# Kernel optimization log

Measured on AMD Instinct MI355X. Metric: run time of the kernel, lower is better.

Reference implementation:

```python
import jax, jax.numpy as jnp
import numpy as np

D_MODEL = 1024
N_HEADS = 16
D_HEAD = D_MODEL // N_HEADS
D_FF = 4096
EPS = 1e-5


def layernorm(x, gamma, beta):
    mu = jnp.mean(x, axis=-1, keepdims=True)
    var = jnp.var(x, axis=-1, keepdims=True)
    return (x - mu) * jax.lax.rsqrt(var + EPS) * gamma + beta


def setup_inputs() -> dict:
    key = jax.random.key(0)
    ks = jax.random.split(key, 16)
    B, T = 4, 2048
    s = 1.0 / np.sqrt(D_MODEL)
    sf = 1.0 / np.sqrt(D_FF)
    return {
        "x": jax.random.normal(ks[0], (B, T, D_MODEL), jnp.float32),
        "gate_score": jax.random.uniform(ks[1], (B,), jnp.float32),
        "Wq": jax.random.normal(ks[2], (D_MODEL, D_MODEL), jnp.float32) * s,
        "bq": jnp.zeros((D_MODEL,), jnp.float32),
        "Wk": jax.random.normal(ks[3], (D_MODEL, D_MODEL), jnp.float32) * s,
        "bk": jnp.zeros((D_MODEL,), jnp.float32),
        "Wv": jax.random.normal(ks[4], (D_MODEL, D_MODEL), jnp.float32) * s,
        "bv": jnp.zeros((D_MODEL,), jnp.float32),
        "Wo": jax.random.normal(ks[5], (D_MODEL, D_MODEL), jnp.float32) * s,
        "bo": jnp.zeros((D_MODEL,), jnp.float32),
        "W1": jax.random.normal(ks[6], (D_MODEL, D_FF), jnp.float32) * s,
        "b1": jnp.zeros((D_FF,), jnp.float32),
        "W2": jax.random.normal(ks[7], (D_FF, D_MODEL), jnp.float32) * sf,
        "b2": jnp.zeros((D_MODEL,), jnp.float32),
        "gamma1": jnp.ones((D_MODEL,), jnp.float32),
        "beta1": jnp.zeros((D_MODEL,), jnp.float32),
        "gamma2": jnp.ones((D_MODEL,), jnp.float32),
        "beta2": jnp.zeros((D_MODEL,), jnp.float32),
    }


def reference(x, gate_score, Wq, bq, Wk, bk, Wv, bv, Wo, bo,
              W1, b1, W2, b2, gamma1, beta1, gamma2, beta2):
    B, T, C = x.shape
    # --- attention sub-block (pre-norm) ---
    h = layernorm(x, gamma1, beta1)
    Q = (h @ Wq + bq).reshape(B, T, N_HEADS, D_HEAD).transpose(0, 2, 1, 3)
    K = (h @ Wk + bk).reshape(B, T, N_HEADS, D_HEAD).transpose(0, 2, 1, 3)
    V = (h @ Wv + bv).reshape(B, T, N_HEADS, D_HEAD).transpose(0, 2, 1, 3)
    scores = jnp.einsum("bhqd,bhkd->bhqk", Q, K) / np.sqrt(D_HEAD)
    causal = jnp.tril(jnp.ones((T, T), dtype=bool))  # True = keep
    scores = jnp.where(causal, scores, -jnp.inf)
    attn = jax.nn.softmax(scores, axis=-1)
    ctx = jnp.einsum("bhqk,bhkd->bhqd", attn, V)
    ctx = ctx.transpose(0, 2, 1, 3).reshape(B, T, C)
    attn_out = ctx @ Wo + bo
    x1 = x + attn_out
    # --- FFN sub-block (pre-norm) ---
    h2 = layernorm(x1, gamma2, beta2)
    ff = jax.nn.gelu(h2 @ W1 + b1, approximate=False) @ W2 + b2
    x2 = x1 + ff
    # --- gated residual ---
    g = gate_score[:, None, None]
    return x + g * (x2 - x)
```

## Files before the change

kernel.cpp:

```cpp
#include <hip/hip_runtime.h>
#include <hip/hip_bf16.h>
#include <cmath>

typedef unsigned short u16;
typedef __attribute__((ext_vector_type(8))) short short8;
typedef __attribute__((ext_vector_type(4))) float f32x4;

#define DM 1024
#define NH 16
#define DH 64
#define DFF 4096
#define BB 4
#define TT 2048
#define MROWS (BB*TT)

__device__ __forceinline__ float bu2f(u16 u) {
    union { float f; unsigned v; } c; c.v = ((unsigned)u) << 16; return c.f;
}
__device__ __forceinline__ u16 f2bu(float f) {
    __hip_bfloat16 h = __float2bfloat16(f);
    union { __hip_bfloat16 h; u16 u; } c; c.h = h; return c.u;
}
__device__ __forceinline__ void async_copy16(const u16* g, u16* l) {
    __builtin_amdgcn_global_load_lds((const __attribute__((address_space(1))) void*)g,
                                     (__attribute__((address_space(3))) void*)l, 16, 0, 0);
}

__global__ void ln_kernel(const float* __restrict__ x, const float* __restrict__ gamma,
                          const float* __restrict__ beta, u16* __restrict__ out)
{
    int row = blockIdx.x;
    int tid = threadIdx.x;
    float4 v4 = ((const float4*)(x + (size_t)row * DM))[tid];
    float v[4] = { v4.x, v4.y, v4.z, v4.w };
    float s = v[0] + v[1] + v[2] + v[3];
    float ss = v[0]*v[0] + v[1]*v[1] + v[2]*v[2] + v[3]*v[3];
    #pragma unroll
    for (int o = 32; o > 0; o >>= 1) { s += __shfl_down(s, o); ss += __shfl_down(ss, o); }
    __shared__ float red[8];
    int w = tid >> 6;
    if ((tid & 63) == 0) { red[w] = s; red[4 + w] = ss; }
    __syncthreads();
    s  = red[0] + red[1] + red[2] + red[3];
    ss = red[4] + red[5] + red[6] + red[7];
    float mu  = s * (1.0f / DM);
    float var = ss * (1.0f / DM) - mu * mu;
    float rstd = rsqrtf(var + 1e-5f);
    float4 g4 = ((const float4*)gamma)[tid];
    float4 b4 = ((const float4*)beta)[tid];
    float g[4] = { g4.x, g4.y, g4.z, g4.w };
    float b[4] = { b4.x, b4.y, b4.z, b4.w };
    ushort4 o4;
    u16* op = (u16*)&o4;
    #pragma unroll
    for (int i = 0; i < 4; i++) op[i] = f2bu((v[i] - mu) * rstd * g[i] + b[i]);
    ((ushort4*)(out + (size_t)row * DM))[tid] = o4;
}

__global__ void transpose4_f2b(const float* __restrict__ w0, const float* __restrict__ w1,
                               const float* __restrict__ w2, const float* __restrict__ w3,
                               u16* __restrict__ outQKV, u16* __restrict__ outO)
{
    __shared__ u16 tile[32][33];
    const float* in = (blockIdx.z == 0) ? w0 : (blockIdx.z == 1) ? w1
                     : (blockIdx.z == 2) ? w2 : w3;
    u16* out = (blockIdx.z < 3) ? (outQKV + (size_t)blockIdx.z * DM * DM) : outO;
    int bx = blockIdx.x * 32;
    int by = blockIdx.y * 32;
    int tx = threadIdx.x, ty = threadIdx.y;
    #pragma unroll
    for (int i = 0; i < 32; i += 8)
        tile[ty + i][tx] = f2bu(in[(size_t)(by + ty + i) * DM + bx + tx]);
    __syncthreads();
    #pragma unroll
    for (int i = 0; i < 32; i += 8)
        out[(size_t)(bx + ty + i) * DM + by + tx] = tile[tx][ty + i];
}

__global__ void transpose_f2b(const float* __restrict__ in, u16* __restrict__ out,
                              int R, int C)
{
    __shared__ u16 tile[32][33];
    int bx = blockIdx.x * 32;
    int by = blockIdx.y * 32;
    int tx = threadIdx.x, ty = threadIdx.y;
    #pragma unroll
    for (int i = 0; i < 32; i += 8)
        tile[ty + i][tx] = f2bu(in[(size_t)(by + ty + i) * C + bx + tx]);
    __syncthreads();
    #pragma unroll
    for (int i = 0; i < 32; i += 8)
        out[(size_t)(bx + ty + i) * R + by + tx] = tile[tx][ty + i];
}

#define BM 128
#define BN 128
#define BK 64

template<int EPI>
__global__ void gemm_bt(
    const u16* __restrict__ A, const u16* __restrict__ Bt,
    const float* __restrict__ bias, const float* __restrict__ bias2,
    const float* __restrict__ bias3, void* __restrict__ Cv,
    const float* __restrict__ res, const float* __restrict__ x0,
    const float* __restrict__ gate, int M, int N, int K)
{
    __shared__ __align__(16) u16 As[BM * BK];
    __shared__ __align__(16) u16 Bs[BN * BK];
    int tid = threadIdx.x;
    int lane = tid & 63, wave = tid >> 6;
    int wm = (wave & 1) * 64, wn = (wave >> 1) * 64;
    int lm = lane & 15, quad = lane >> 4;
    size_t row0 = (size_t)blockIdx.x * BM;
    size_t col0 = (size_t)blockIdx.y * BN;

    int sr = tid >> 3;
    int scol = (((tid & 7) ^ (sr & 7)) * 8);
    const u16* Ag = A  + (row0 + sr) * (size_t)K + scol;
    const u16* Bg = Bt + (col0 + sr) * (size_t)K + scol;
    u16* Asl = As + tid * 8;
    u16* Bsl = Bs + tid * 8;

    int fc0 = ((0 * 4 + quad) ^ (lm & 7)) * 8;
    int fc1 = ((1 * 4 + quad) ^ (lm & 7)) * 8;

    f32x4 acc[4][4];
    #pragma unroll
    for (int i = 0; i < 4; i++)
        #pragma unroll
        for (int j = 0; j < 4; j++)
            acc[i][j] = (f32x4){0.f, 0.f, 0.f, 0.f};

    for (int k0 = 0; k0 < K; k0 += BK) {
        __syncthreads();
        async_copy16(Ag + k0,                  Asl);
        async_copy16(Ag + (size_t)32 * K + k0, Asl + 32 * BK);
        async_copy16(Ag + (size_t)64 * K + k0, Asl + 64 * BK);
        async_copy16(Ag + (size_t)96 * K + k0, Asl + 96 * BK);
        async_copy16(Bg + k0,                  Bsl);
        async_copy16(Bg + (size_t)32 * K + k0, Bsl + 32 * BK);
        async_copy16(Bg + (size_t)64 * K + k0, Bsl + 64 * BK);
        async_copy16(Bg + (size_t)96 * K + k0, Bsl + 96 * BK);
        __syncthreads();
        #pragma unroll
        for (int ks = 0; ks < 2; ks++) {
            int fc = ks ? fc1 : fc0;
            short8 af[4], bfr[4];
            #pragma unroll
            for (int t = 0; t < 4; t++) {
                af[t]  = *(const short8*)&As[(wm + t * 16 + lm) * BK + fc];
                bfr[t] = *(const short8*)&Bs[(wn + t * 16 + lm) * BK + fc];
            }
            #pragma unroll
            for (int mt = 0; mt < 4; mt++)
                #pragma unroll
                for (int nt = 0; nt < 4; nt++)
                    acc[mt][nt] = __builtin_amdgcn_mfma_f32_16x16x32_bf16(
                        af[mt], bfr[nt], acc[mt][nt], 0, 0, 0);
        }
    }

    u16*   C16 = (u16*)Cv;
    float* Cf  = (float*)Cv;

    const float* bb = bias;
    size_t csub = 0;
    if (EPI == 0 && bias2 != nullptr) {
        size_t cbase = col0 + wn;
        if (cbase >= 2048)      { bb = bias3; csub = 2048; }
        else if (cbase >= 1024) { bb = bias2; csub = 1024; }
    }

    #pragma unroll
    for (int mt = 0; mt < 4; mt++) {
        #pragma unroll
        for (int nt = 0; nt < 4; nt++) {
            #pragma unroll
            for (int r = 0; r < 4; r++) {
                size_t row = row0 + wm + mt * 16 + quad * 4 + r;
                size_t col = col0 + wn + nt * 16 + lm;
                size_t idx = row * (size_t)N + col;
                float v = acc[mt][nt][r] + bb[col - csub];
                if (EPI == 0) {
                    C16[idx] = f2bu(v);
                } else if (EPI == 1) {
                    Cf[idx] = v + res[idx];
                } else if (EPI == 2) {
                    v = 0.5f * v * (1.0f + erff(v * 0.70710678118f));
                    C16[idx] = f2bu(v);
                } else {
                    float xv  = x0[idx];
                    float x1v = res[idx];
                    float g   = gate[row >> 11];
                    Cf[idx] = xv + g * (x1v + v - xv);
                }
            }
        }
    }
}

#define BM2 256
#define BN2 256
#define BK2 64

template<int EPI>
__global__ __launch_bounds__(512, 2) void gemm_bt256(
    const u16* __restrict__ A, const u16* __restrict__ Bt,
    const float* __restrict__ bias, const float* __restrict__ bias2,
    const float* __restrict__ bias3, void* __restrict__ Cv,
    int M, int N, int K)
{
    __shared__ __align__(16) u16 LA[2][2][128][64];
    __shared__ __align__(16) u16 LB[2][2][128][64];

    int tid = threadIdx.x;
    int lane = tid & 63, wave = tid >> 6;
    int wm = wave >> 2, wn = wave & 3;
    int lm = lane & 15, quad = lane >> 4;

    size_t row0 = (size_t)blockIdx.x * BM2;
    size_t col0 = (size_t)blockIdx.y * BN2;

    int srow = wave * 8 + (lane >> 3);
    int scol = ((lane & 7) ^ ((lane >> 3) & 7)) * 8;
    const u16* Ag = A  + (row0 + srow) * (size_t)K + scol;
    const u16* Bg = Bt + (col0 + srow) * (size_t)K + scol;

    int fc0 = (quad ^ (lm & 7)) * 8;
    int fc1 = ((4 + quad) ^ (lm & 7)) * 8;

    f32x4 acc[8][4];
    #pragma unroll
    for (int i = 0; i < 8; i++)
        #pragma unroll
        for (int j = 0; j < 4; j++)
            acc[i][j] = (f32x4){0.f, 0.f, 0.f, 0.f};

    const int NT = K / BK2;

    async_copy16(Ag,                   &LA[0][0][0][0]  + tid * 8);
    async_copy16(Ag + (size_t)64 * K,  &LA[0][0][64][0] + tid * 8);
    async_copy16(Bg,                   &LB[0][0][0][0]  + tid * 8);
    async_copy16(Bg + (size_t)64 * K,  &LB[0][0][64][0] + tid * 8);
    async_copy16(Bg + (size_t)128 * K, &LB[0][1][0][0]  + tid * 8);
    async_copy16(Bg + (size_t)192 * K, &LB[0][1][64][0] + tid * 8);
    async_copy16(Ag + (size_t)128 * K, &LA[0][1][0][0]  + tid * 8);
    async_copy16(Ag + (size_t)192 * K, &LA[0][1][64][0] + tid * 8);
    asm volatile("s_waitcnt vmcnt(4)" ::: "memory");
    __builtin_amdgcn_s_barrier();
    __builtin_amdgcn_sched_barrier(0);

    for (int t = 0; t < NT; ++t) {
        int cur = t & 1, nb = cur ^ 1;
        bool hn = (t + 1 < NT);
        size_t koff = (size_t)(t + 1) * BK2;

        short8 af[4][2], bf[2][2], bg[2][2];

        #pragma unroll
        for (int mf = 0; mf < 4; mf++) {
            af[mf][0] = *(const short8*)&LA[cur][0][wm * 64 + mf * 16 + lm][fc0];
            af[mf][1] = *(const short8*)&LA[cur][0][wm * 64 + mf * 16 + lm][fc1];
        }
        #pragma unroll
        for (int nf = 0; nf < 2; nf++) {
            bf[nf][0] = *(const short8*)&LB[cur][0][wn * 32 + nf * 16 + lm][fc0];
            bf[nf][1] = *(const short8*)&LB[cur][0][wn * 32 + nf * 16 + lm][fc1];
        }
        if (hn) {
            async_copy16(Ag + koff,                   &LA[nb][0][0][0]  + tid * 8);
            async_copy16(Ag + (size_t)64 * K + koff,  &LA[nb][0][64][0] + tid * 8);
            asm volatile("s_waitcnt vmcnt(4)" ::: "memory");
        } else {
            asm volatile("s_waitcnt vmcnt(2)" ::: "memory");
        }
        __builtin_amdgcn_s_barrier();
        __builtin_amdgcn_sched_barrier(0);
        __builtin_amdgcn_s_setprio(1);
        #pragma unroll
        for (int mf = 0; mf < 4; mf++)
            #pragma unroll
            for (int nf = 0; nf < 2; nf++) {
                acc[mf][nf] = __builtin_amdgcn_mfma_f32_16x16x32_bf16(af[mf][0], bf[nf][0], acc[mf][nf], 0, 0, 0);
                acc[mf][nf] = __builtin_amdgcn_mfma_f32_16x16x32_bf16(af[mf][1], bf[nf][1], acc[mf][nf], 0, 0, 0);
            }
        __builtin_amdgcn_s_setprio(0);
        __builtin_amdgcn_s_barrier();
        __builtin_amdgcn_sched_barrier(0);

        #pragma unroll
        for (int nf = 0; nf < 2; nf++) {
            bg[nf][0] = *(const short8*)&LB[cur][1][wn * 32 + nf * 16 + lm][fc0];
            bg[nf][1] = *(const short8*)&LB[cur][1][wn * 32 + nf * 16 + lm][fc1];
        }
        if (hn) {
            async_copy16(Bg + koff,                   &LB[nb][0][0][0]  + tid * 8);
            async_copy16(Bg + (size_t)64 * K + koff,  &LB[nb][0][64][0] + tid * 8);
            asm volatile("s_waitcnt vmcnt(4)" ::: "memory");
        } else {
            asm volatile("s_waitcnt vmcnt(0)" ::: "memory");
        }
        __builtin_amdgcn_s_barrier();
        __builtin_amdgcn_sched_barrier(0);
        __builtin_amdgcn_s_setprio(1);
        #pragma unroll
        for (int mf = 0; mf < 4; mf++)
            #pragma unroll
            for (int nf = 0; nf < 2; nf++) {
                acc[mf][2 + nf] = __builtin_amdgcn_mfma_f32_16x16x32_bf16(af[mf][0], bg[nf][0], acc[mf][2 + nf], 0, 0, 0);
                acc[mf][2 + nf] = __builtin_amdgcn_mfma_f32_16x16x32_bf16(af[mf][1], bg[nf][1], acc[mf][2 + nf], 0, 0, 0);
            }
        __builtin_amdgcn_s_setprio(0);
        __builtin_amdgcn_s_barrier();
        __builtin_amdgcn_sched_barrier(0);

        #pragma unroll
        for (int mf = 0; mf < 4; mf++) {
            af[mf][0] = *(const short8*)&LA[cur][1][wm * 64 + mf * 16 + lm][fc0];
            af[mf][1] = *(const short8*)&LA[cur][1][wm * 64 + mf * 16 + lm][fc1];
        }
        if (hn) {
            async_copy16(Bg + (size_t)128 * K + koff, &LB[nb][1][0][0]  + tid * 8);
            async_copy16(Bg + (size_t)192 * K + koff, &LB[nb][1][64][0] + tid * 8);
        }
        __builtin_amdgcn_s_barrier();
        __builtin_amdgcn_sched_barrier(0);
        __builtin_amdgcn_s_setprio(1);
        #pragma unroll
        for (int mf = 0; mf < 4; mf++)
            #pragma unroll
            for (int nf = 0; nf < 2; nf++) {
                acc[4 + mf][2 + nf] = __builtin_amdgcn_mfma_f32_16x16x32_bf16(af[mf][0], bg[nf][0], acc[4 + mf][2 + nf], 0, 0, 0);
                acc[4 + mf][2 + nf] = __builtin_amdgcn_mfma_f32_16x16x32_bf16(af[mf][1], bg[nf][1], acc[4 + mf][2 + nf], 0, 0, 0);
            }
        __builtin_amdgcn_s_setprio(0);
        __builtin_amdgcn_s_barrier();
        __builtin_amdgcn_sched_barrier(0);

        #pragma unroll
        for (int nf = 0; nf < 2; nf++) {
            bf[nf][0] = *(const short8*)&LB[cur][0][wn * 32 + nf * 16 + lm][fc0];
            bf[nf][1] = *(const short8*)&LB[cur][0][wn * 32 + nf * 16 + lm][fc1];
        }
        if (hn) {
            async_copy16(Ag + (size_t)128 * K + koff, &LA[nb][1][0][0]  + tid * 8);
            async_copy16(Ag + (size_t)192 * K + koff, &LA[nb][1][64][0] + tid * 8);
            asm volatile("s_waitcnt vmcnt(4)" ::: "memory");
        }
        __builtin_amdgcn_s_barrier();
        __builtin_amdgcn_sched_barrier(0);
        __builtin_amdgcn_s_setprio(1);
        #pragma unroll
        for (int mf = 0; mf < 4; mf++)
            #pragma unroll
            for (int nf = 0; nf < 2; nf++) {
                acc[4 + mf][nf] = __builtin_amdgcn_mfma_f32_16x16x32_bf16(af[mf][0], bf[nf][0], acc[4 + mf][nf], 0, 0, 0);
                acc[4 + mf][nf] = __builtin_amdgcn_mfma_f32_16x16x32_bf16(af[mf][1], bf[nf][1], acc[4 + mf][nf], 0, 0, 0);
            }
        __builtin_amdgcn_s_setprio(0);
        __builtin_amdgcn_s_barrier();
        __builtin_amdgcn_sched_barrier(0);
    }

    u16* C16 = (u16*)Cv;
    const float* bb = bias;
    size_t csub = 0;
    if (EPI == 0 && bias2 != nullptr) {
        if (col0 >= 2048)      { bb = bias3; csub = 2048; }
        else if (col0 >= 1024) { bb = bias2; csub = 1024; }
    }
    #pragma unroll
    for (int mq = 0; mq < 8; mq++) {
        #pragma unroll
        for (int nq = 0; nq < 4; nq++) {
            #pragma unroll
            for (int r = 0; r < 4; r++) {
                size_t row = row0 + (size_t)(mq >> 2) * 128 + wm * 64 + (mq & 3) * 16 + quad * 4 + r;
                size_t col = col0 + (size_t)(nq >> 1) * 128 + wn * 32 + (nq & 1) * 16 + lm;
                float v = acc[mq][nq][r] + bb[col - csub];
                if (EPI == 2)
                    v = 0.5f * v * (1.0f + erff(v * 0.70710678118f));
                C16[row * (size_t)N + col] = f2bu(v);
            }
        }
    }
}

#define AVS 72

__global__ __launch_bounds__(256, 4) void attn_mfma(
    const u16* __restrict__ QKV, u16* __restrict__ ctx)
{
    __shared__ __align__(16) u16 Kl[64][AVS];
    __shared__ __align__(16) u16 Vt[64][AVS];
    __shared__ __align__(16) u16 Pl[4][16][AVS];

    const int LD = 3 * DM;
    int tid = threadIdx.x, lane = tid & 63, w = tid >> 6;
    int lm = lane & 15, quad = lane >> 4;

    int bi = blockIdx.x;
    int pair = bi & 15, h = (bi >> 4) & 15, b = bi >> 8;
    int t1 = 31 - pair, t2 = pair;

    const size_t hoff = (size_t)h * DH;
    const u16* Qp = QKV + (size_t)b * TT * LD + hoff;
    const u16* Kp = Qp + DM;
    const u16* Vp = Qp + 2 * DM;

    short8 aqA[2], aqB[2];
    #pragma unroll
    for (int dc = 0; dc < 2; dc++) {
        aqA[dc] = *(const short8*)(Qp + (size_t)(t1 * 64 + w * 16 + lm) * LD + dc * 32 + quad * 8);
        aqB[dc] = *(const short8*)(Qp + (size_t)(t2 * 64 + w * 16 + lm) * LD + dc * 32 + quad * 8);
    }

    int kkey = tid & 63, kdim = (tid >> 6) * 16;
    int vkey = (tid & 31) * 2, vdim = (tid >> 5) * 8;

    const u16* kb0 = Kp + (size_t)kkey * LD + kdim;
    const u16* vb0 = Vp + (size_t)vkey * LD + vdim;
    const u16* vb1 = Vp + (size_t)(vkey + 1) * LD + vdim;

    const float sc = 0.18033688011f;
    const float FM = 24.0f;
    const short s1 = (short)0x3F80;
    const short8 ones = (short8){s1, s1, s1, s1, s1, s1, s1, s1};

    uint4 kr0 = *(const uint4*)(kb0);
    uint4 kr1 = *(const uint4*)(kb0 + 8);
    uint4 vr0 = *(const uint4*)(vb0);
    uint4 vr1 = *(const uint4*)(vb1);

    #pragma unroll
    for (int ti = 0; ti < 2; ti++) {
        int tcur = (ti == 0) ? t1 : t2;
        int nch = tcur + 1;
        int q0 = tcur * 64;
        int qw = q0 + w * 16;
        short8 a0 = (ti == 0) ? aqA[0] : aqB[0];
        short8 a1 = (ti == 0) ? aqA[1] : aqB[1];
        int qv = qw + lm;

        f32x4 o[4], o5;
        #pragma unroll
        for (int ds = 0; ds < 4; ds++) o[ds] = (f32x4){0.f, 0.f, 0.f, 0.f};
        o5 = (f32x4){0.f, 0.f, 0.f, 0.f};

        for (int c = 0; c < nch; c++) {
            int kb = c * 64;
            __syncthreads();
            *(uint4*)&Kl[kkey][kdim]     = kr0;
            *(uint4*)&Kl[kkey][kdim + 8] = kr1;
            {
                const u16* p0 = (const u16*)&vr0;
                const u16* p1 = (const u16*)&vr1;
                #pragma unroll
                for (int j = 0; j < 8; j++) {
                    ushort2 pk = { p0[j], p1[j] };
                    *(ushort2*)&Vt[vdim + j][vkey] = pk;
                }
            }
            __syncthreads();

            {
                size_t offn = (c + 1 < nch) ? (size_t)(c + 1) * 64 * LD : 0;
                kr0 = *(const uint4*)(kb0 + offn);
                kr1 = *(const uint4*)(kb0 + offn + 8);
                vr0 = *(const uint4*)(vb0 + offn);
                vr1 = *(const uint4*)(vb1 + offn);
            }

            f32x4 s[4];
            #pragma unroll
            for (int ks = 0; ks < 4; ks++) s[ks] = (f32x4){0.f, 0.f, 0.f, 0.f};
            #pragma unroll
            for (int ks = 0; ks < 4; ks++) {
                short8 k0 = *(const short8*)&Kl[ks * 16 + lm][quad * 8];
                short8 k1 = *(const short8*)&Kl[ks * 16 + lm][32 + quad * 8];
                s[ks] = __builtin_amdgcn_mfma_f32_16x16x32_bf16(k0, a0, s[ks], 0, 0, 0);
                s[ks] = __builtin_amdgcn_mfma_f32_16x16x32_bf16(k1, a1, s[ks], 0, 0, 0);
            }

            bool mz = (kb + 63 > qw);
            #pragma unroll
            for (int ks = 0; ks < 4; ks++) {
                int kbase = kb + ks * 16 + quad * 4;
                ushort4 pk;
                u16* pp = (u16*)&pk;
                #pragma unroll
                for (int r = 0; r < 4; r++) {
                    float v = s[ks][r] * sc - FM;
                    if (mz && (kbase + r > qv)) v = -INFINITY;
                    pp[r] = f2bu(exp2f(v));
                }
                *(ushort4*)&Pl[w][lm][ks * 16 + quad * 4] = pk;
            }

            #pragma unroll
            for (int kc = 0; kc < 2; kc++) {
                short8 ap = *(const short8*)&Pl[w][lm][kc * 32 + quad * 8];
                #pragma unroll
                for (int ds = 0; ds < 4; ds++) {
                    short8 bv = *(const short8*)&Vt[ds * 16 + lm][kc * 32 + quad * 8];
                    o[ds] = __builtin_amdgcn_mfma_f32_16x16x32_bf16(ap, bv, o[ds], 0, 0, 0);
                }
                o5 = __builtin_amdgcn_mfma_f32_16x16x32_bf16(ap, ones, o5, 0, 0, 0);
            }
        }

        float inv[4];
        #pragma unroll
        for (int r = 0; r < 4; r++) inv[r] = 1.0f / o5[r];
        #pragma unroll
        for (int ds = 0; ds < 4; ds++)
            #pragma unroll
            for (int r = 0; r < 4; r++) {
                size_t row = (size_t)(b * TT + qw + quad * 4 + r);
                ctx[row * DM + hoff + ds * 16 + lm] = f2bu(o[ds][r] * inv[r]);
            }
    }
}

extern "C" void kernel_launch(void* const* d_in, const int* in_sizes, int n_in,
                              void* d_out, int out_size, void* d_ws, size_t ws_size,
                              hipStream_t stream)
{
    const float* x    = (const float*)d_in[0];
    const float* gate = (const float*)d_in[1];
    const float* Wq   = (const float*)d_in[2];
    const float* bq   = (const float*)d_in[3];
    const float* Wk   = (const float*)d_in[4];
    const float* bk   = (const float*)d_in[5];
    const float* Wv   = (const float*)d_in[6];
    const float* bv   = (const float*)d_in[7];
    const float* Wo   = (const float*)d_in[8];
    const float* bo   = (const float*)d_in[9];
    const float* W1   = (const float*)d_in[10];
    const float* b1   = (const float*)d_in[11];
    const float* W2   = (const float*)d_in[12];
    const float* b2   = (const float*)d_in[13];
    const float* gamma1 = (const float*)d_in[14];
    const float* beta1  = (const float*)d_in[15];
    const float* gamma2 = (const float*)d_in[16];
    const float* beta2  = (const float*)d_in[17];
    float* out = (float*)d_out;

    char* ws = (char*)d_ws;
    const size_t MB = 1024 * 1024;
    u16* WtQKV = (u16*)(ws + 0 * MB);
    u16* WtO   = (u16*)(ws + 6 * MB);
    u16* Wt1   = (u16*)(ws + 8 * MB);
    u16* Wt2   = (u16*)(ws + 16 * MB);
    u16* h     = (u16*)(ws + 24 * MB);
    u16* ctx   = (u16*)(ws + 24 * MB);
    u16* QKVb  = (u16*)(ws + 40 * MB);
    float* x1  = (float*)(ws + 40 * MB);
    u16* h2    = (u16*)(ws + 72 * MB);
    u16* ff    = (u16*)(ws + 88 * MB);

    dim3 tb(32, 8);
    transpose4_f2b<<<dim3(32, 32, 4), tb, 0, stream>>>(Wq, Wk, Wv, Wo, WtQKV, WtO);
    transpose_f2b<<<dim3(DFF / 32, DM / 32), tb, 0, stream>>>(W1, Wt1, DM, DFF);
    transpose_f2b<<<dim3(DM / 32, DFF / 32), tb, 0, stream>>>(W2, Wt2, DFF, DM);

    ln_kernel<<<MROWS, 256, 0, stream>>>(x, gamma1, beta1, h);

    gemm_bt256<0><<<dim3(MROWS / BM2, 3 * DM / BN2), 512, 0, stream>>>(
        h, WtQKV, bq, bk, bv, QKVb, MROWS, 3 * DM, DM);

    attn_mfma<<<BB * NH * 16, 256, 0, stream>>>(QKVb, ctx);

    gemm_bt<1><<<dim3(MROWS / BM, DM / BN), 256, 0, stream>>>(
        ctx, WtO, bo, nullptr, nullptr, x1, x, nullptr, nullptr, MROWS, DM, DM);

    ln_kernel<<<MROWS, 256, 0, stream>>>(x1, gamma2, beta2, h2);

    gemm_bt256<2><<<dim3(MROWS / BM2, DFF / BN2), 512, 0, stream>>>(
        h2, Wt1, b1, nullptr, nullptr, ff, MROWS, DFF, DM);

    gemm_bt<3><<<dim3(MROWS / BM, DM / BN), 256, 0, stream>>>(
        ff, Wt2, b2, nullptr, nullptr, out, x1, x, gate, MROWS, DM, DFF);
}
```

Measured before the change: 552.3 us.

## Restructure 256-tile GEMM barriers and split attention into one q-tile per block

The 256x256 GEMM main loop drops the trailing barrier after each MFMA group, waits on LDS reads explicitly before compute, and reuses the already-loaded B fragments in the last quadrant instead of reloading them from LDS. The attention kernel stops pairing a long and a short causal q-tile in one block and launches twice as many blocks with one tile each. It also changes the LDS row pad from 72 to 66 and raises the occupancy hint to 6 blocks. A dead bias-selection branch is removed from the 128 GEMM. Fewer barriers and more blocks aim to raise overlap and occupancy, but dropping barriers risks LDS races between waves, and per-block work in attention becomes unbalanced (the launch order starts with the longest tiles).

```diff
diff --git a/kernel.cpp b/kernel.cpp
--- a/kernel.cpp
+++ b/kernel.cpp
@@ -165,11 +165,6 @@
 
     const float* bb = bias;
     size_t csub = 0;
-    if (EPI == 0 && bias2 != nullptr) {
-        size_t cbase = col0 + wn;
-        if (cbase >= 2048)      { bb = bias3; csub = 2048; }
-        else if (cbase >= 1024) { bb = bias2; csub = 1024; }
-    }
 
     #pragma unroll
     for (int mt = 0; mt < 4; mt++) {
@@ -203,6 +198,19 @@
 #define BN2 256
 #define BK2 64
 
+#define MFMA16(ACC, MB, NB, AF, BF)                                                 \
+    do {                                                                            \
+        _Pragma("unroll")                                                           \
+        for (int mf = 0; mf < 4; mf++)                                              \
+            _Pragma("unroll")                                                       \
+            for (int nf = 0; nf < 2; nf++) {                                        \
+                ACC[(MB) + mf][(NB) + nf] = __builtin_amdgcn_mfma_f32_16x16x32_bf16( \
+                    AF[mf][0], BF[nf][0], ACC[(MB) + mf][(NB) + nf], 0, 0, 0);      \
+                ACC[(MB) + mf][(NB) + nf] = __builtin_amdgcn_mfma_f32_16x16x32_bf16( \
+                    AF[mf][1], BF[nf][1], ACC[(MB) + mf][(NB) + nf], 0, 0, 0);      \
+            }                                                                       \
+    } while (0)
+
 template<int EPI>
 __global__ __launch_bounds__(512, 2) void gemm_bt256(
     const u16* __restrict__ A, const u16* __restrict__ Bt,
@@ -228,6 +236,8 @@
 
     int fc0 = (quad ^ (lm & 7)) * 8;
     int fc1 = ((4 + quad) ^ (lm & 7)) * 8;
+    int arow = wm * 64 + lm;
+    int brow = wn * 32 + lm;
 
     f32x4 acc[8][4];
     #pragma unroll
@@ -248,100 +258,73 @@
     async_copy16(Ag + (size_t)192 * K, &LA[0][1][64][0] + tid * 8);
     asm volatile("s_waitcnt vmcnt(4)" ::: "memory");
     __builtin_amdgcn_s_barrier();
-    __builtin_amdgcn_sched_barrier(0);
+
+    short8 af[4][2], bf[2][2], bg2[2][2];
 
     for (int t = 0; t < NT; ++t) {
         int cur = t & 1, nb = cur ^ 1;
         bool hn = (t + 1 < NT);
         size_t koff = (size_t)(t + 1) * BK2;
 
-        short8 af[4][2], bf[2][2], bg[2][2];
-
         #pragma unroll
         for (int mf = 0; mf < 4; mf++) {
-            af[mf][0] = *(const short8*)&LA[cur][0][wm * 64 + mf * 16 + lm][fc0];
-            af[mf][1] = *(const short8*)&LA[cur][0][wm * 64 + mf * 16 + lm][fc1];
+            af[mf][0] = *(const short8*)&LA[cur][0][arow + mf * 16][fc0];
+            af[mf][1] = *(const short8*)&LA[cur][0][arow + mf * 16][fc1];
         }
         #pragma unroll
         for (int nf = 0; nf < 2; nf++) {
-            bf[nf][0] = *(const short8*)&LB[cur][0][wn * 32 + nf * 16 + lm][fc0];
-            bf[nf][1] = *(const short8*)&LB[cur][0][wn * 32 + nf * 16 + lm][fc1];
+            bf[nf][0] = *(const short8*)&LB[cur][0][brow + nf * 16][fc0];
+            bf[nf][1] = *(const short8*)&LB[cur][0][brow + nf * 16][fc1];
         }
         if (hn) {
-            async_copy16(Ag + koff,                   &LA[nb][0][0][0]  + tid * 8);
-            async_copy16(Ag + (size_t)64 * K + koff,  &LA[nb][0][64][0] + tid * 8);
+            async_copy16(Ag + koff,                  &LA[nb][0][0][0]  + tid * 8);
+            async_copy16(Ag + (size_t)64 * K + koff, &LA[nb][0][64][0] + tid * 8);
             asm volatile("s_waitcnt vmcnt(4)" ::: "memory");
         } else {
             asm volatile("s_waitcnt vmcnt(2)" ::: "memory");
         }
         __builtin_amdgcn_s_barrier();
+        asm volatile("s_waitcnt lgkmcnt(0)" ::: "memory");
         __builtin_amdgcn_sched_barrier(0);
         __builtin_amdgcn_s_setprio(1);
-        #pragma unroll
-        for (int mf = 0; mf < 4; mf++)
-            #pragma unroll
-            for (int nf = 0; nf < 2; nf++) {
-                acc[mf][nf] = __builtin_amdgcn_mfma_f32_16x16x32_bf16(af[mf][0], bf[nf][0], acc[mf][nf], 0, 0, 0);
-                acc[mf][nf] = __builtin_amdgcn_mfma_f32_16x16x32_bf16(af[mf][1], bf[nf][1], acc[mf][nf], 0, 0, 0);
-            }
+        MFMA16(acc, 0, 0, af, bf);
         __builtin_amdgcn_s_setprio(0);
-        __builtin_amdgcn_s_barrier();
-        __builtin_amdgcn_sched_barrier(0);
 
         #pragma unroll
         for (int nf = 0; nf < 2; nf++) {
-            bg[nf][0] = *(const short8*)&LB[cur][1][wn * 32 + nf * 16 + lm][fc0];
-            bg[nf][1] = *(const short8*)&LB[cur][1][wn * 32 + nf * 16 + lm][fc1];
+            bg2[nf][0] = *(const short8*)&LB[cur][1][brow + nf * 16][fc0];
+            bg2[nf][1] = *(const short8*)&LB[cur][1][brow + nf * 16][fc1];
         }
         if (hn) {
-            async_copy16(Bg + koff,                   &LB[nb][0][0][0]  + tid * 8);
-            async_copy16(Bg + (size_t)64 * K + koff,  &LB[nb][0][64][0] + tid * 8);
+            async_copy16(Bg + koff,                  &LB[nb][0][0][0]  + tid * 8);
+            async_copy16(Bg + (size_t)64 * K + koff, &LB[nb][0][64][0] + tid * 8);
             asm volatile("s_waitcnt vmcnt(4)" ::: "memory");
         } else {
             asm volatile("s_waitcnt vmcnt(0)" ::: "memory");
         }
         __builtin_amdgcn_s_barrier();
+        asm volatile("s_waitcnt lgkmcnt(0)" ::: "memory");
         __builtin_amdgcn_sched_barrier(0);
         __builtin_amdgcn_s_setprio(1);
-        #pragma unroll
-        for (int mf = 0; mf < 4; mf++)
-            #pragma unroll
-            for (int nf = 0; nf < 2; nf++) {
-                acc[mf][2 + nf] = __builtin_amdgcn_mfma_f32_16x16x32_bf16(af[mf][0], bg[nf][0], acc[mf][2 + nf], 0, 0, 0);
-                acc[mf][2 + nf] = __builtin_amdgcn_mfma_f32_16x16x32_bf16(af[mf][1], bg[nf][1], acc[mf][2 + nf], 0, 0, 0);
-            }
+        MFMA16(acc, 0, 2, af, bg2);
         __builtin_amdgcn_s_setprio(0);
-        __builtin_amdgcn_s_barrier();
-        __builtin_amdgcn_sched_barrier(0);
 
         #pragma unroll
         for (int mf = 0; mf < 4; mf++) {
-            af[mf][0] = *(const short8*)&LA[cur][1][wm * 64 + mf * 16 + lm][fc0];
-            af[mf][1] = *(const short8*)&LA[cur][1][wm * 64 + mf * 16 + lm][fc1];
+            af[mf][0] = *(const short8*)&LA[cur][1][arow + mf * 16][fc0];
+            af[mf][1] = *(const short8*)&LA[cur][1][arow + mf * 16][fc1];
         }
         if (hn) {
             async_copy16(Bg + (size_t)128 * K + koff, &LB[nb][1][0][0]  + tid * 8);
             async_copy16(Bg + (size_t)192 * K + koff, &LB[nb][1][64][0] + tid * 8);
         }
         __builtin_amdgcn_s_barrier();
+        asm volatile("s_waitcnt lgkmcnt(0)" ::: "memory");
         __builtin_amdgcn_sched_barrier(0);
         __builtin_amdgcn_s_setprio(1);
-        #pragma unroll
-        for (int mf = 0; mf < 4; mf++)
-            #pragma unroll
-            for (int nf = 0; nf < 2; nf++) {
-                acc[4 + mf][2 + nf] = __builtin_amdgcn_mfma_f32_16x16x32_bf16(af[mf][0], bg[nf][0], acc[4 + mf][2 + nf], 0, 0, 0);
-                acc[4 + mf][2 + nf] = __builtin_amdgcn_mfma_f32_16x16x32_bf16(af[mf][1], bg[nf][1], acc[4 + mf][2 + nf], 0, 0, 0);
-            }
+        MFMA16(acc, 4, 2, af, bg2);
         __builtin_amdgcn_s_setprio(0);
-        __builtin_amdgcn_s_barrier();
-        __builtin_amdgcn_sched_barrier(0);
-
-        #pragma unroll
-        for (int nf = 0; nf < 2; nf++) {
-            bf[nf][0] = *(const short8*)&LB[cur][0][wn * 32 + nf * 16 + lm][fc0];
-            bf[nf][1] = *(const short8*)&LB[cur][0][wn * 32 + nf * 16 + lm][fc1];
-        }
+
         if (hn) {
             async_copy16(Ag + (size_t)128 * K + koff, &LA[nb][1][0][0]  + tid * 8);
             async_copy16(Ag + (size_t)192 * K + koff, &LA[nb][1][64][0] + tid * 8);
@@ -350,16 +333,8 @@
         __builtin_amdgcn_s_barrier();
         __builtin_amdgcn_sched_barrier(0);
         __builtin_amdgcn_s_setprio(1);
-        #pragma unroll
-        for (int mf = 0; mf < 4; mf++)
-            #pragma unroll
-            for (int nf = 0; nf < 2; nf++) {
-                acc[4 + mf][nf] = __builtin_amdgcn_mfma_f32_16x16x32_bf16(af[mf][0], bf[nf][0], acc[4 + mf][nf], 0, 0, 0);
-                acc[4 + mf][nf] = __builtin_amdgcn_mfma_f32_16x16x32_bf16(af[mf][1], bf[nf][1], acc[4 + mf][nf], 0, 0, 0);
-            }
+        MFMA16(acc, 4, 0, af, bf);
         __builtin_amdgcn_s_setprio(0);
-        __builtin_amdgcn_s_barrier();
-        __builtin_amdgcn_sched_barrier(0);
     }
 
     u16* C16 = (u16*)Cv;
@@ -370,25 +345,31 @@
         else if (col0 >= 1024) { bb = bias2; csub = 1024; }
     }
     #pragma unroll
-    for (int mq = 0; mq < 8; mq++) {
-        #pragma unroll
-        for (int nq = 0; nq < 4; nq++) {
-            #pragma unroll
-            for (int r = 0; r < 4; r++) {
-                size_t row = row0 + (size_t)(mq >> 2) * 128 + wm * 64 + (mq & 3) * 16 + quad * 4 + r;
-                size_t col = col0 + (size_t)(nq >> 1) * 128 + wn * 32 + (nq & 1) * 16 + lm;
-                float v = acc[mq][nq][r] + bb[col - csub];
-                if (EPI == 2)
-                    v = 0.5f * v * (1.0f + erff(v * 0.70710678118f));
-                C16[row * (size_t)N + col] = f2bu(v);
+    for (int mq = 0; mq < 2; mq++) {
+        #pragma unroll
+        for (int mf = 0; mf < 4; mf++) {
+            #pragma unroll
+            for (int nq = 0; nq < 2; nq++) {
+                #pragma unroll
+                for (int nf = 0; nf < 2; nf++) {
+                    #pragma unroll
+                    for (int r = 0; r < 4; r++) {
+                        size_t row = row0 + (size_t)mq * 128 + wm * 64 + mf * 16 + quad * 4 + r;
+                        size_t col = col0 + (size_t)nq * 128 + wn * 32 + nf * 16 + lm;
+                        float v = acc[mq * 4 + mf][nq * 2 + nf][r] + bb[col - csub];
+                        if (EPI == 2)
+                            v = 0.5f * v * (1.0f + erff(v * 0.70710678118f));
+                        C16[row * (size_t)N + col] = f2bu(v);
+                    }
+                }
             }
         }
     }
 }
 
-#define AVS 72
-
-__global__ __launch_bounds__(256, 4) void attn_mfma(
+#define AVS 66
+
+__global__ __launch_bounds__(256, 6) void attn_mfma(
     const u16* __restrict__ QKV, u16* __restrict__ ctx)
 {
     __shared__ __align__(16) u16 Kl[64][AVS];
@@ -400,20 +381,20 @@
     int lm = lane & 15, quad = lane >> 4;
 
     int bi = blockIdx.x;
-    int pair = bi & 15, h = (bi >> 4) & 15, b = bi >> 8;
-    int t1 = 31 - pair, t2 = pair;
+    int t = 31 - (bi & 31);
+    int h = (bi >> 5) & 15, b = bi >> 9;
 
     const size_t hoff = (size_t)h * DH;
     const u16* Qp = QKV + (size_t)b * TT * LD + hoff;
     const u16* Kp = Qp + DM;
     const u16* Vp = Qp + 2 * DM;
 
-    short8 aqA[2], aqB[2];
-    #pragma unroll
-    for (int dc = 0; dc < 2; dc++) {
-        aqA[dc] = *(const short8*)(Qp + (size_t)(t1 * 64 + w * 16 + lm) * LD + dc * 32 + quad * 8);
-        aqB[dc] = *(const short8*)(Qp + (size_t)(t2 * 64 + w * 16 + lm) * LD + dc * 32 + quad * 8);
-    }
+    int q0 = t * 64;
+    int qw = q0 + w * 16;
+    int qv = qw + lm;
+
+    short8 a0 = *(const short8*)(Qp + (size_t)(qw + lm) * LD + quad * 8);
+    short8 a1 = *(const short8*)(Qp + (size_t)(qw + lm) * LD + 32 + quad * 8);
 
     int kkey = tid & 63, kdim = (tid >> 6) * 16;
     int vkey = (tid & 31) * 2, vdim = (tid >> 5) * 8;
@@ -432,94 +413,84 @@
     uint4 vr0 = *(const uint4*)(vb0);
     uint4 vr1 = *(const uint4*)(vb1);
 
-    #pragma unroll
-    for (int ti = 0; ti < 2; ti++) {
-        int tcur = (ti == 0) ? t1 : t2;
-        int nch = tcur + 1;
-        int q0 = tcur * 64;
-        int qw = q0 + w * 16;
-        short8 a0 = (ti == 0) ? aqA[0] : aqB[0];
-        short8 a1 = (ti == 0) ? aqA[1] : aqB[1];
-        int qv = qw + lm;
-
-        f32x4 o[4], o5;
-        #pragma unroll
-        for (int ds = 0; ds < 4; ds++) o[ds] = (f32x4){0.f, 0.f, 0.f, 0.f};
-        o5 = (f32x4){0.f, 0.f, 0.f, 0.f};
-
-        for (int c = 0; c < nch; c++) {
-            int kb = c * 64;
-            __syncthreads();
-            *(uint4*)&Kl[kkey][kdim]     = kr0;
-            *(uint4*)&Kl[kkey][kdim + 8] = kr1;
-            {
-                const u16* p0 = (const u16*)&vr0;
-                const u16* p1 = (const u16*)&vr1;
-                #pragma unroll
-                for (int j = 0; j < 8; j++) {
-                    ushort2 pk = { p0[j], p1[j] };
-                    *(ushort2*)&Vt[vdim + j][vkey] = pk;
-                }
+    f32x4 o[4], o5;
+    #pragma unroll
+    for (int ds = 0; ds < 4; ds++) o[ds] = (f32x4){0.f, 0.f, 0.f, 0.f};
+    o5 = (f32x4){0.f, 0.f, 0.f, 0.f};
+
+    int nch = t + 1;
+    for (int c = 0; c < nch; c++) {
+        int kb = c * 64;
+        __syncthreads();
+        *(uint4*)&Kl[kkey][kdim]     = kr0;
+        *(uint4*)&Kl[kkey][kdim + 8] = kr1;
+        {
+            const u16* p0 = (const u16*)&vr0;
+            const u16* p1 = (const u16*)&vr1;
+            #pragma unroll
+            for (int j = 0; j < 8; j++) {
+                ushort2 pk = { p0[j], p1[j] };
+                *(ushort2*)&Vt[vdim + j][vkey] = pk;
             }
-            __syncthreads();
-
-            {
-                size_t offn = (c + 1 < nch) ? (size_t)(c + 1) * 64 * LD : 0;
-                kr0 = *(const uint4*)(kb0 + offn);
-                kr1 = *(const uint4*)(kb0 + offn + 8);
-                vr0 = *(const uint4*)(vb0 + offn);
-                vr1 = *(const uint4*)(vb1 + offn);
+        }
+        __syncthreads();
+
+        {
+            size_t offn = (c + 1 < nch) ? (size_t)(c + 1) * 64 * LD : 0;
+            kr0 = *(const uint4*)(kb0 + offn);
+            kr1 = *(const uint4*)(kb0 + offn + 8);
+            vr0 = *(const uint4*)(vb0 + offn);
+            vr1 = *(const uint4*)(vb1 + offn);
+        }
+
+        f32x4 s[4];
+        #pragma unroll
+        for (int ks = 0; ks < 4; ks++) s[ks] = (f32x4){0.f, 0.f, 0.f, 0.f};
+        #pragma unroll
+        for (int ks = 0; ks < 4; ks++) {
+            short8 k0 = *(const short8*)&Kl[ks * 16 + lm][quad * 8];
+            short8 k1 = *(const short8*)&Kl[ks * 16 + lm][32 + quad * 8];
+            s[ks] = __builtin_amdgcn_mfma_f32_16x16x32_bf16(k0, a0, s[ks], 0, 0, 0);
+            s[ks] = __builtin_amdgcn_mfma_f32_16x16x32_bf16(k1, a1, s[ks], 0, 0, 0);
+        }
+
+        bool mz = (kb + 63 > qw);
+        #pragma unroll
+        for (int ks = 0; ks < 4; ks++) {
+            int kbase = kb + ks * 16 + quad * 4;
+            ushort4 pk;
+            u16* pp = (u16*)&pk;
+            #pragma unroll
+            for (int r = 0; r < 4; r++) {
+                float v = s[ks][r] * sc - FM;
+                if (mz && (kbase + r > qv)) v = -INFINITY;
+                pp[r] = f2bu(exp2f(v));
             }
-
-            f32x4 s[4];
-            #pragma unroll
-            for (int ks = 0; ks < 4; ks++) s[ks] = (f32x4){0.f, 0.f, 0.f, 0.f};
-            #pragma unroll
-            for (int ks = 0; ks < 4; ks++) {
-                short8 k0 = *(const short8*)&Kl[ks * 16 + lm][quad * 8];
-                short8 k1 = *(const short8*)&Kl[ks * 16 + lm][32 + quad * 8];
-                s[ks] = __builtin_amdgcn_mfma_f32_16x16x32_bf16(k0, a0, s[ks], 0, 0, 0);
-                s[ks] = __builtin_amdgcn_mfma_f32_16x16x32_bf16(k1, a1, s[ks], 0, 0, 0);
+            *(ushort4*)&Pl[w][lm][ks * 16 + quad * 4] = pk;
+        }
+
+        #pragma unroll
+        for (int kc = 0; kc < 2; kc++) {
+            short8 ap = *(const short8*)&Pl[w][lm][kc * 32 + quad * 8];
+            #pragma unroll
+            for (int ds = 0; ds < 4; ds++) {
+                short8 bv = *(const short8*)&Vt[ds * 16 + lm][kc * 32 + quad * 8];
+                o[ds] = __builtin_amdgcn_mfma_f32_16x16x32_bf16(ap, bv, o[ds], 0, 0, 0);
             }
-
-            bool mz = (kb + 63 > qw);
-            #pragma unroll
-            for (int ks = 0; ks < 4; ks++) {
-                int kbase = kb + ks * 16 + quad * 4;
-                ushort4 pk;
-                u16* pp = (u16*)&pk;
-                #pragma unroll
-                for (int r = 0; r < 4; r++) {
-                    float v = s[ks][r] * sc - FM;
-                    if (mz && (kbase + r > qv)) v = -INFINITY;
-                    pp[r] = f2bu(exp2f(v));
-                }
-                *(ushort4*)&Pl[w][lm][ks * 16 + quad * 4] = pk;
-            }
-
-            #pragma unroll
-            for (int kc = 0; kc < 2; kc++) {
-                short8 ap = *(const short8*)&Pl[w][lm][kc * 32 + quad * 8];
-                #pragma unroll
-                for (int ds = 0; ds < 4; ds++) {
-                    short8 bv = *(const short8*)&Vt[ds * 16 + lm][kc * 32 + quad * 8];
-                    o[ds] = __builtin_amdgcn_mfma_f32_16x16x32_bf16(ap, bv, o[ds], 0, 0, 0);
-                }
-                o5 = __builtin_amdgcn_mfma_f32_16x16x32_bf16(ap, ones, o5, 0, 0, 0);
-            }
-        }
-
-        float inv[4];
-        #pragma unroll
-        for (int r = 0; r < 4; r++) inv[r] = 1.0f / o5[r];
-        #pragma unroll
-        for (int ds = 0; ds < 4; ds++)
-            #pragma unroll
-            for (int r = 0; r < 4; r++) {
-                size_t row = (size_t)(b * TT + qw + quad * 4 + r);
-                ctx[row * DM + hoff + ds * 16 + lm] = f2bu(o[ds][r] * inv[r]);
-            }
+            o5 = __builtin_amdgcn_mfma_f32_16x16x32_bf16(ap, ones, o5, 0, 0, 0);
+        }
     }
+
+    float inv[4];
+    #pragma unroll
+    for (int r = 0; r < 4; r++) inv[r] = 1.0f / o5[r];
+    #pragma unroll
+    for (int ds = 0; ds < 4; ds++)
+        #pragma unroll
+        for (int r = 0; r < 4; r++) {
+            size_t row = (size_t)(b * TT + qw + quad * 4 + r);
+            ctx[row * DM + hoff + ds * 16 + lm] = f2bu(o[ds][r] * inv[r]);
+        }
 }
 
 extern "C" void kernel_launch(void* const* d_in, const int* in_sizes, int n_in,
@@ -569,7 +540,7 @@
     gemm_bt256<0><<<dim3(MROWS / BM2, 3 * DM / BN2), 512, 0, stream>>>(
         h, WtQKV, bq, bk, bv, QKVb, MROWS, 3 * DM, DM);
 
-    attn_mfma<<<BB * NH * 16, 256, 0, stream>>>(QKVb, ctx);
+    attn_mfma<<<BB * NH * 32, 256, 0, stream>>>(QKVb, ctx);
 
     gemm_bt<1><<<dim3(MROWS / BM, DM / BN), 256, 0, stream>>>(
         ctx, WtO, bo, nullptr, nullptr, x1, x, nullptr, nullptr, MROWS, DM, DM);
```

New measurement: 616.3 us. 1.12x slower.
